# Kernel optimization log

Measured on AMD Instinct MI355X. Metric: run time of the kernel, lower is better.

The kernel has to match this reference:

```python
import jax, jax.numpy as jnp
import numpy as np

B, N, C = 4, 2048, 1024
H = 16
D = C // H  # head_dim = 64
SCALE = 1.0 / np.sqrt(D).astype(np.float32)


def setup_inputs() -> dict:
    key = jax.random.key(0)
    ks = jax.random.split(key, 6)
    s = 0.02
    return {
        "x": jax.random.normal(ks[0], (B, N, C), dtype=jnp.float32),
        "Wq": jax.random.normal(ks[1], (C, C), dtype=jnp.float32) * s,
        "Wk": jax.random.normal(ks[2], (C, C), dtype=jnp.float32) * s,
        "Wv": jax.random.normal(ks[3], (C, C), dtype=jnp.float32) * s,
        "Wo": jax.random.normal(ks[4], (C, C), dtype=jnp.float32) * s,
        "bo": jax.random.normal(ks[5], (C,), dtype=jnp.float32) * s,
    }


def reference(x, Wq, Wk, Wv, Wo, bo):
    # q/k/v projections (no bias, qkv_bias=False), split heads -> [B,H,N,D]
    def heads(t):
        return t.reshape(B, N, H, D).transpose(0, 2, 1, 3)
    q = heads(x @ Wq)
    k = heads(x @ Wk)
    v = heads(x @ Wv)
    attn = jnp.einsum("bhnd,bhmd->bhnm", q, k) * SCALE  # [B,H,N,N]
    attn = jax.nn.softmax(attn, axis=-1)
    out = jnp.einsum("bhnm,bhmd->bhnd", attn, v)  # [B,H,N,D]
    out = out.transpose(0, 2, 1, 3).reshape(B, N, C)
    return out @ Wo + bo
```

## Files before the change

### kernel.cpp

```cpp
#include <hip/hip_runtime.h>
#include <hip/hip_bf16.h>


typedef __bf16 bf16x8 __attribute__((ext_vector_type(8)));
typedef float  f32x4  __attribute__((ext_vector_type(4)));
typedef unsigned int u32x4 __attribute__((ext_vector_type(4)));

__device__ __forceinline__ f32x4 mfma16(bf16x8 a, bf16x8 b, f32x4 c) {
    return __builtin_amdgcn_mfma_f32_16x16x32_bf16(a, b, c, 0, 0, 0);
}

__device__ __forceinline__ unsigned short f2bf(float f) {
    unsigned u = __builtin_bit_cast(unsigned, f);
    u += 0x7fffu + ((u >> 16) & 1u);
    return (unsigned short)(u >> 16);
}

__device__ __forceinline__ unsigned cvt_pk_bf16(float lo, float hi) {
    unsigned r;
    asm("v_cvt_pk_bf16_f32 %0, %1, %2" : "=v"(r) : "v"(lo), "v"(hi));
    return r;
}

__device__ __forceinline__ void gload16(const ushort* g, ushort* l) {
    __builtin_amdgcn_global_load_lds(
        (const __attribute__((address_space(1))) void*)g,
        (__attribute__((address_space(3))) void*)l, 16, 0, 0);
}

__global__ void cast_bf16_kernel(const float4* __restrict__ in,
                                 ushort4* __restrict__ out, int n4) {
    int i = blockIdx.x * blockDim.x + threadIdx.x;
    if (i < n4) {
        float4 f = in[i];
        ushort4 r;
        r.x = f2bf(f.x); r.y = f2bf(f.y); r.z = f2bf(f.z); r.w = f2bf(f.w);
        out[i] = r;
    }
}

__global__ void transpose_cast_kernel(const float* __restrict__ Wq,
                                      const float* __restrict__ Wk,
                                      const float* __restrict__ Wv,
                                      const float* __restrict__ Wo,
                                      ushort* __restrict__ out) {
    __shared__ float tile[32][33];
    const int z = blockIdx.z;
    const float* W = (z == 0) ? Wq : (z == 1) ? Wk : (z == 2) ? Wv : Wo;
    ushort* o = out + (size_t)z * 1024 * 1024;
    const int k0 = blockIdx.x * 32, n0 = blockIdx.y * 32;
    const int tx = threadIdx.x, ty = threadIdx.y;
#pragma unroll
    for (int i = 0; i < 4; i++)
        tile[ty + 8 * i][tx] = W[(size_t)(k0 + ty + 8 * i) * 1024 + n0 + tx];
    __syncthreads();
#pragma unroll
    for (int i = 0; i < 4; i++)
        o[(size_t)(n0 + ty + 8 * i) * 1024 + k0 + tx] = f2bf(tile[tx][ty + 8 * i]);
}

template <int MODE>
__global__ __launch_bounds__(256) void gemm128(const ushort* __restrict__ A,
                                               const ushort* __restrict__ Bt,
                                               ushort* __restrict__ outB,
                                               float* __restrict__ outF,
                                               const float* __restrict__ bias) {
    __shared__ ushort As[128 * 32];
    __shared__ ushort Bs[128 * 32];
    const int tid = threadIdx.x;
    const int lane = tid & 63;
    const int wid = tid >> 6;
    const int wm = wid >> 1, wn = wid & 1;
    const int m0 = blockIdx.x * 128;
    const int n0 = blockIdx.y * 128;
    if (MODE == 0) Bt += (size_t)blockIdx.z * (1024 * 1024);

    f32x4 acc[4][4] = {};

    for (int k0 = 0; k0 < 1024; k0 += 32) {
#pragma unroll
        for (int it = 0; it < 2; ++it) {
            int e = (it * 256 + tid) * 8;
            int r = e >> 5, c = e & 31;
            gload16(&A[(size_t)(m0 + r) * 1024 + k0 + c], &As[e]);
            gload16(&Bt[(size_t)(n0 + r) * 1024 + k0 + c], &Bs[e]);
        }
        __syncthreads();

        bf16x8 a[4], b[4];
#pragma unroll
        for (int i = 0; i < 4; i++) {
            a[i] = *(const bf16x8*)&As[(wm * 64 + i * 16 + (lane & 15)) * 32 + (lane >> 4) * 8];
            b[i] = *(const bf16x8*)&Bs[(wn * 64 + i * 16 + (lane & 15)) * 32 + (lane >> 4) * 8];
        }
#pragma unroll
        for (int i = 0; i < 4; i++)
#pragma unroll
            for (int j = 0; j < 4; j++)
                acc[i][j] = mfma16(a[i], b[j], acc[i][j]);
        __syncthreads();
    }

#pragma unroll
    for (int i = 0; i < 4; i++) {
        int row_b = m0 + wm * 64 + i * 16 + ((lane >> 4) * 4);
#pragma unroll
        for (int j = 0; j < 4; j++) {
            int col = n0 + wn * 64 + j * 16 + (lane & 15);
#pragma unroll
            for (int r = 0; r < 4; r++) {
                int row = row_b + r;
                float v = acc[i][j][r];
                if (MODE == 0) {
                    ushort* o = outB + (size_t)blockIdx.z * (8192ull * 1024);
                    int b = row >> 11, n = row & 2047, h = col >> 6, d = col & 63;
                    o[((((size_t)(b * 16 + h)) * 2048 + n) << 6) + d] = f2bf(v);
                } else {
                    outF[(size_t)row * 1024 + col] = v + bias[col];
                }
            }
        }
    }
}

#define LSCALE 0.18033688f

__global__ __launch_bounds__(256) void attn_kernel(const ushort* __restrict__ Q,
                                                   const ushort* __restrict__ K,
                                                   const ushort* __restrict__ V,
                                                   ushort* __restrict__ O) {
    __shared__ ushort Ks[64 * 64];
    __shared__ ushort Vs[64 * 64];
    __shared__ ushort Ps[4][16 * 64];
    const int tid = threadIdx.x;
    const int lane = tid & 63;
    const int wid = tid >> 6;
    const int g = lane >> 4;
    const int q16 = lane & 15;
    const int qt = blockIdx.x;
    const int bh = blockIdx.y;
    const size_t base = (size_t)bh * (2048 * 64);

    const int qrow = qt * 64 + wid * 16 + q16;
    bf16x8 qf[2];
    qf[0] = *(const bf16x8*)&Q[base + (size_t)qrow * 64 + g * 8];
    qf[1] = *(const bf16x8*)&Q[base + (size_t)qrow * 64 + 32 + g * 8];

    bf16x8 onesb;
#pragma unroll
    for (int i = 0; i < 8; i++) onesb[i] = (__bf16)1.0f;

    f32x4 o[4] = {};
    f32x4 lacc = {};
    float m_run = -1e30f;

    char* KsB = (char*)Ks;
    char* VsB = (char*)Vs;
    char* PsB = (char*)Ps[wid];

    for (int kt = 0; kt < 2048; kt += 64) {
#pragma unroll
        for (int it = 0; it < 2; ++it) {
            int ci = it * 256 + tid;
            int key = ci >> 3, d0 = (ci & 7) * 8;
            uint4 kv = *(const uint4*)&K[base + (size_t)(kt + key) * 64 + d0];
            int byt = (key * 128 + d0 * 2) ^ ((key & 7) << 4);
            *(uint4*)(KsB + byt) = kv;

            int key2 = ci & 63;
            int d0v = (ci >> 6) * 8;
            uint4 vv = *(const uint4*)&V[base + (size_t)(kt + key2) * 64 + d0v];
            const ushort* vs = (const ushort*)&vv;
#pragma unroll
            for (int j = 0; j < 8; j++) {
                int d = d0v + j;
                int b2 = (d * 128 + key2 * 2) ^ ((d & 7) << 4);
                *(ushort*)(VsB + b2) = vs[j];
            }
        }
        __syncthreads();

        f32x4 s[4] = {};
#pragma unroll
        for (int kb = 0; kb < 4; ++kb) {
#pragma unroll
            for (int ks = 0; ks < 2; ++ks) {
                int key = kb * 16 + q16;
                int d0 = ks * 32 + g * 8;
                int byt = (key * 128 + d0 * 2) ^ ((key & 7) << 4);
                bf16x8 kf = *(const bf16x8*)(KsB + byt);
                s[kb] = mfma16(kf, qf[ks], s[kb]);
            }
        }

        float t[4][4];
#pragma unroll
        for (int kb = 0; kb < 4; ++kb)
#pragma unroll
            for (int r = 0; r < 4; ++r) t[kb][r] = s[kb][r] * LSCALE;

        float mx = fmaxf(fmaxf(fmaxf(t[0][0], t[0][1]), fmaxf(t[0][2], t[0][3])),
                         fmaxf(fmaxf(t[1][0], t[1][1]), fmaxf(t[1][2], t[1][3])));
        mx = fmaxf(mx, fmaxf(fmaxf(fmaxf(t[2][0], t[2][1]), fmaxf(t[2][2], t[2][3])),
                             fmaxf(fmaxf(t[3][0], t[3][1]), fmaxf(t[3][2], t[3][3]))));
        mx = fmaxf(mx, __shfl_xor(mx, 16));
        mx = fmaxf(mx, __shfl_xor(mx, 32));
        float mn = fmaxf(m_run, mx);
        float fr = __builtin_amdgcn_exp2f(m_run - mn);
        m_run = mn;

        unsigned w[4][2];
#pragma unroll
        for (int kb = 0; kb < 4; ++kb) {
            float p0 = __builtin_amdgcn_exp2f(t[kb][0] - mn);
            float p1 = __builtin_amdgcn_exp2f(t[kb][1] - mn);
            float p2 = __builtin_amdgcn_exp2f(t[kb][2] - mn);
            float p3 = __builtin_amdgcn_exp2f(t[kb][3] - mn);
            w[kb][0] = cvt_pk_bf16(p0, p1);
            w[kb][1] = cvt_pk_bf16(p2, p3);
        }

        {
            u32x4 c0 = {w[0][0], w[0][1], w[2][0], w[2][1]};
            u32x4 c1 = {w[1][0], w[1][1], w[3][0], w[3][1]};
            *(u32x4*)(PsB + ((lane * 32 + 0)  ^ ((lane & 7) << 4))) = c0;
            *(u32x4*)(PsB + ((lane * 32 + 16) ^ ((lane & 7) << 4))) = c1;
        }
        int s1 = q16 + 32 * (g & 1);
        int ch = (g >> 1) * 16;
        u32x4 r1 = *(const u32x4*)(PsB + ((s1 * 32 + ch) ^ ((s1 & 7) << 4)));
        u32x4 r2 = *(const u32x4*)(PsB + (((s1 + 16) * 32 + ch) ^ (((s1 + 16) & 7) << 4)));
        bf16x8 pa[2];
        {
            u32x4 p0 = {r1.x, r1.y, r2.x, r2.y};
            u32x4 p1 = {r1.z, r1.w, r2.z, r2.w};
            pa[0] = __builtin_bit_cast(bf16x8, p0);
            pa[1] = __builtin_bit_cast(bf16x8, p1);
        }

        float fro[4];
#pragma unroll
        for (int r = 0; r < 4; ++r) fro[r] = __shfl(fr, g * 4 + r);
#pragma unroll
        for (int cb = 0; cb < 4; ++cb)
#pragma unroll
            for (int r = 0; r < 4; ++r) o[cb][r] *= fro[r];
#pragma unroll
        for (int r = 0; r < 4; ++r) lacc[r] *= fro[r];

        lacc = mfma16(pa[0], onesb, lacc);
        lacc = mfma16(pa[1], onesb, lacc);

#pragma unroll
        for (int cb = 0; cb < 4; ++cb) {
#pragma unroll
            for (int ks = 0; ks < 2; ++ks) {
                int d = cb * 16 + q16;
                int byt = (d * 128 + (ks * 32 + g * 8) * 2) ^ ((d & 7) << 4);
                bf16x8 vf = *(const bf16x8*)(VsB + byt);
                o[cb] = mfma16(pa[ks], vf, o[cb]);
            }
        }
        __syncthreads();
    }

    const int b = bh >> 4, h = bh & 15;
#pragma unroll
    for (int r = 0; r < 4; ++r) {
        float inv = 1.0f / lacc[r];
        int row = qt * 64 + wid * 16 + g * 4 + r;
#pragma unroll
        for (int cb = 0; cb < 4; ++cb) {
            int col = h * 64 + cb * 16 + q16;
            O[((size_t)(b * 2048 + row)) * 1024 + col] = f2bf(o[cb][r] * inv);
        }
    }
}

extern "C" void kernel_launch(void* const* d_in, const int* in_sizes, int n_in,
                              void* d_out, int out_size, void* d_ws, size_t ws_size,
                              hipStream_t stream) {
    const float* x  = (const float*)d_in[0];
    const float* Wq = (const float*)d_in[1];
    const float* Wk = (const float*)d_in[2];
    const float* Wv = (const float*)d_in[3];
    const float* Wo = (const float*)d_in[4];
    const float* bo = (const float*)d_in[5];
    float* out = (float*)d_out;

    if (ws_size < (size_t)72 * 1024 * 1024) return;
    ushort* ws  = (ushort*)d_ws;
    ushort* xb  = ws;
    ushort* wt  = xb + (size_t)8 * 1024 * 1024;
    ushort* qkv = wt + (size_t)4 * 1024 * 1024;
    ushort* ao  = xb;

    cast_bf16_kernel<<<8192, 256, 0, stream>>>((const float4*)x, (ushort4*)xb,
                                               2 * 1024 * 1024);
    transpose_cast_kernel<<<dim3(32, 32, 4), dim3(32, 8), 0, stream>>>(Wq, Wk, Wv, Wo, wt);
    gemm128<0><<<dim3(64, 8, 3), 256, 0, stream>>>(xb, wt, qkv, nullptr, nullptr);
    attn_kernel<<<dim3(32, 64), 256, 0, stream>>>(
        qkv, qkv + (size_t)8 * 1024 * 1024, qkv + (size_t)16 * 1024 * 1024, ao);
    gemm128<1><<<dim3(64, 8, 1), 256, 0, stream>>>(ao, wt + (size_t)3 * 1024 * 1024,
                                                   nullptr, out, bo);
}
```

Baseline: 260.0 us.

## Process two 16-row query tiles per wave and swizzle attention block order

Each wave now handles 32 query rows (two 16-row sub-tiles), so every K/V tile staged in shared memory feeds twice as many MFMAs. This halves the number of K/V global loads and LDS staging passes per query row. The grid shrinks to 1024 blocks, and block IDs are remapped so that blocks resident together spread across heads, which is meant to improve cache locality. The cost is more accumulator registers per thread, which may reduce occupancy.

Result: faster. 250.0 us (-3.8%).

```diff
diff --git a/kernel.cpp b/kernel.cpp
--- a/kernel.cpp
+++ b/kernel.cpp
@@ -131,32 +131,36 @@
                                                    ushort* __restrict__ O) {
     __shared__ ushort Ks[64 * 64];
     __shared__ ushort Vs[64 * 64];
-    __shared__ ushort Ps[4][16 * 64];
+    __shared__ ushort Ps[4][2][1024];
     const int tid = threadIdx.x;
     const int lane = tid & 63;
     const int wid = tid >> 6;
     const int g = lane >> 4;
     const int q16 = lane & 15;
-    const int qt = blockIdx.x;
-    const int bh = blockIdx.y;
+    const int bid = blockIdx.x;
+    const int swz = (bid & 7) * 128 + (bid >> 3);
+    const int bh = swz >> 4;
+    const int qt = swz & 15;
     const size_t base = (size_t)bh * (2048 * 64);
 
-    const int qrow = qt * 64 + wid * 16 + q16;
-    bf16x8 qf[2];
-    qf[0] = *(const bf16x8*)&Q[base + (size_t)qrow * 64 + g * 8];
-    qf[1] = *(const bf16x8*)&Q[base + (size_t)qrow * 64 + 32 + g * 8];
+    const int qr0 = qt * 128 + wid * 32 + q16;
+    bf16x8 qf[2][2];
+#pragma unroll
+    for (int u = 0; u < 2; ++u)
+#pragma unroll
+        for (int ks = 0; ks < 2; ++ks)
+            qf[u][ks] = *(const bf16x8*)&Q[base + (size_t)(qr0 + u * 16) * 64 + ks * 32 + g * 8];
 
     bf16x8 onesb;
 #pragma unroll
     for (int i = 0; i < 8; i++) onesb[i] = (__bf16)1.0f;
 
-    f32x4 o[4] = {};
-    f32x4 lacc = {};
-    float m_run = -1e30f;
+    f32x4 o[2][4] = {};
+    f32x4 lacc[2] = {};
+    float m_run[2] = {-1e30f, -1e30f};
 
     char* KsB = (char*)Ks;
     char* VsB = (char*)Vs;
-    char* PsB = (char*)Ps[wid];
 
     for (int kt = 0; kt < 2048; kt += 64) {
 #pragma unroll
@@ -180,7 +184,7 @@
         }
         __syncthreads();
 
-        f32x4 s[4] = {};
+        f32x4 s[2][4] = {};
 #pragma unroll
         for (int kb = 0; kb < 4; ++kb) {
 #pragma unroll
@@ -189,67 +193,75 @@
                 int d0 = ks * 32 + g * 8;
                 int byt = (key * 128 + d0 * 2) ^ ((key & 7) << 4);
                 bf16x8 kf = *(const bf16x8*)(KsB + byt);
-                s[kb] = mfma16(kf, qf[ks], s[kb]);
-            }
-        }
-
-        float t[4][4];
-#pragma unroll
-        for (int kb = 0; kb < 4; ++kb)
-#pragma unroll
-            for (int r = 0; r < 4; ++r) t[kb][r] = s[kb][r] * LSCALE;
-
-        float mx = fmaxf(fmaxf(fmaxf(t[0][0], t[0][1]), fmaxf(t[0][2], t[0][3])),
-                         fmaxf(fmaxf(t[1][0], t[1][1]), fmaxf(t[1][2], t[1][3])));
-        mx = fmaxf(mx, fmaxf(fmaxf(fmaxf(t[2][0], t[2][1]), fmaxf(t[2][2], t[2][3])),
-                             fmaxf(fmaxf(t[3][0], t[3][1]), fmaxf(t[3][2], t[3][3]))));
-        mx = fmaxf(mx, __shfl_xor(mx, 16));
-        mx = fmaxf(mx, __shfl_xor(mx, 32));
-        float mn = fmaxf(m_run, mx);
-        float fr = __builtin_amdgcn_exp2f(m_run - mn);
-        m_run = mn;
-
-        unsigned w[4][2];
-#pragma unroll
-        for (int kb = 0; kb < 4; ++kb) {
-            float p0 = __builtin_amdgcn_exp2f(t[kb][0] - mn);
-            float p1 = __builtin_amdgcn_exp2f(t[kb][1] - mn);
-            float p2 = __builtin_amdgcn_exp2f(t[kb][2] - mn);
-            float p3 = __builtin_amdgcn_exp2f(t[kb][3] - mn);
-            w[kb][0] = cvt_pk_bf16(p0, p1);
-            w[kb][1] = cvt_pk_bf16(p2, p3);
-        }
-
-        {
-            u32x4 c0 = {w[0][0], w[0][1], w[2][0], w[2][1]};
-            u32x4 c1 = {w[1][0], w[1][1], w[3][0], w[3][1]};
-            *(u32x4*)(PsB + ((lane * 32 + 0)  ^ ((lane & 7) << 4))) = c0;
-            *(u32x4*)(PsB + ((lane * 32 + 16) ^ ((lane & 7) << 4))) = c1;
-        }
-        int s1 = q16 + 32 * (g & 1);
-        int ch = (g >> 1) * 16;
-        u32x4 r1 = *(const u32x4*)(PsB + ((s1 * 32 + ch) ^ ((s1 & 7) << 4)));
-        u32x4 r2 = *(const u32x4*)(PsB + (((s1 + 16) * 32 + ch) ^ (((s1 + 16) & 7) << 4)));
-        bf16x8 pa[2];
-        {
-            u32x4 p0 = {r1.x, r1.y, r2.x, r2.y};
-            u32x4 p1 = {r1.z, r1.w, r2.z, r2.w};
-            pa[0] = __builtin_bit_cast(bf16x8, p0);
-            pa[1] = __builtin_bit_cast(bf16x8, p1);
-        }
-
-        float fro[4];
-#pragma unroll
-        for (int r = 0; r < 4; ++r) fro[r] = __shfl(fr, g * 4 + r);
-#pragma unroll
-        for (int cb = 0; cb < 4; ++cb)
-#pragma unroll
-            for (int r = 0; r < 4; ++r) o[cb][r] *= fro[r];
-#pragma unroll
-        for (int r = 0; r < 4; ++r) lacc[r] *= fro[r];
-
-        lacc = mfma16(pa[0], onesb, lacc);
-        lacc = mfma16(pa[1], onesb, lacc);
+                s[0][kb] = mfma16(kf, qf[0][ks], s[0][kb]);
+                s[1][kb] = mfma16(kf, qf[1][ks], s[1][kb]);
+            }
+        }
+
+        bf16x8 pa[2][2];
+#pragma unroll
+        for (int u = 0; u < 2; ++u) {
+            float t[4][4];
+#pragma unroll
+            for (int kb = 0; kb < 4; ++kb)
+#pragma unroll
+                for (int r = 0; r < 4; ++r) t[kb][r] = s[u][kb][r] * LSCALE;
+
+            float mx = fmaxf(fmaxf(fmaxf(t[0][0], t[0][1]), fmaxf(t[0][2], t[0][3])),
+                             fmaxf(fmaxf(t[1][0], t[1][1]), fmaxf(t[1][2], t[1][3])));
+            mx = fmaxf(mx, fmaxf(fmaxf(fmaxf(t[2][0], t[2][1]), fmaxf(t[2][2], t[2][3])),
+                                 fmaxf(fmaxf(t[3][0], t[3][1]), fmaxf(t[3][2], t[3][3]))));
+            mx = fmaxf(mx, __shfl_xor(mx, 16));
+            mx = fmaxf(mx, __shfl_xor(mx, 32));
+            float mn = fmaxf(m_run[u], mx);
+            float fr = __builtin_amdgcn_exp2f(m_run[u] - mn);
+            m_run[u] = mn;
+
+            unsigned w[4][2];
+#pragma unroll
+            for (int kb = 0; kb < 4; ++kb) {
+                float p0 = __builtin_amdgcn_exp2f(t[kb][0] - mn);
+                float p1 = __builtin_amdgcn_exp2f(t[kb][1] - mn);
+                float p2 = __builtin_amdgcn_exp2f(t[kb][2] - mn);
+                float p3 = __builtin_amdgcn_exp2f(t[kb][3] - mn);
+                w[kb][0] = cvt_pk_bf16(p0, p1);
+                w[kb][1] = cvt_pk_bf16(p2, p3);
+            }
+
+            char* PsB = (char*)Ps[wid][u];
+            {
+                u32x4 c0 = {w[0][0], w[0][1], w[2][0], w[2][1]};
+                u32x4 c1 = {w[1][0], w[1][1], w[3][0], w[3][1]};
+                *(u32x4*)(PsB + ((lane * 32 + 0)  ^ ((lane & 7) << 4))) = c0;
+                *(u32x4*)(PsB + ((lane * 32 + 16) ^ ((lane & 7) << 4))) = c1;
+            }
+            asm volatile("" ::: "memory");
+            __builtin_amdgcn_sched_barrier(0);
+            int s1 = q16 + 32 * (g & 1);
+            int ch = (g >> 1) * 16;
+            u32x4 r1 = *(const u32x4*)(PsB + ((s1 * 32 + ch) ^ ((s1 & 7) << 4)));
+            u32x4 r2 = *(const u32x4*)(PsB + (((s1 + 16) * 32 + ch) ^ (((s1 + 16) & 7) << 4)));
+            asm volatile("" ::: "memory");
+            {
+                u32x4 p0 = {r1.x, r1.y, r2.x, r2.y};
+                u32x4 p1 = {r1.z, r1.w, r2.z, r2.w};
+                pa[u][0] = __builtin_bit_cast(bf16x8, p0);
+                pa[u][1] = __builtin_bit_cast(bf16x8, p1);
+            }
+
+            float fro[4];
+#pragma unroll
+            for (int r = 0; r < 4; ++r) fro[r] = __shfl(fr, g * 4 + r);
+#pragma unroll
+            for (int cb = 0; cb < 4; ++cb)
+#pragma unroll
+                for (int r = 0; r < 4; ++r) o[u][cb][r] *= fro[r];
+#pragma unroll
+            for (int r = 0; r < 4; ++r) lacc[u][r] *= fro[r];
+
+            lacc[u] = mfma16(pa[u][0], onesb, lacc[u]);
+            lacc[u] = mfma16(pa[u][1], onesb, lacc[u]);
+        }
 
 #pragma unroll
         for (int cb = 0; cb < 4; ++cb) {
@@ -258,7 +270,8 @@
                 int d = cb * 16 + q16;
                 int byt = (d * 128 + (ks * 32 + g * 8) * 2) ^ ((d & 7) << 4);
                 bf16x8 vf = *(const bf16x8*)(VsB + byt);
-                o[cb] = mfma16(pa[ks], vf, o[cb]);
+                o[0][cb] = mfma16(pa[0][ks], vf, o[0][cb]);
+                o[1][cb] = mfma16(pa[1][ks], vf, o[1][cb]);
             }
         }
         __syncthreads();
@@ -266,13 +279,16 @@
 
     const int b = bh >> 4, h = bh & 15;
 #pragma unroll
-    for (int r = 0; r < 4; ++r) {
-        float inv = 1.0f / lacc[r];
-        int row = qt * 64 + wid * 16 + g * 4 + r;
-#pragma unroll
-        for (int cb = 0; cb < 4; ++cb) {
-            int col = h * 64 + cb * 16 + q16;
-            O[((size_t)(b * 2048 + row)) * 1024 + col] = f2bf(o[cb][r] * inv);
+    for (int u = 0; u < 2; ++u) {
+#pragma unroll
+        for (int r = 0; r < 4; ++r) {
+            float inv = 1.0f / lacc[u][r];
+            int row = qt * 128 + wid * 32 + u * 16 + g * 4 + r;
+#pragma unroll
+            for (int cb = 0; cb < 4; ++cb) {
+                int col = h * 64 + cb * 16 + q16;
+                O[((size_t)(b * 2048 + row)) * 1024 + col] = f2bf(o[u][cb][r] * inv);
+            }
         }
     }
 }
@@ -299,7 +315,7 @@
                                                2 * 1024 * 1024);
     transpose_cast_kernel<<<dim3(32, 32, 4), dim3(32, 8), 0, stream>>>(Wq, Wk, Wv, Wo, wt);
     gemm128<0><<<dim3(64, 8, 3), 256, 0, stream>>>(xb, wt, qkv, nullptr, nullptr);
-    attn_kernel<<<dim3(32, 64), 256, 0, stream>>>(
+    attn_kernel<<<1024, 256, 0, stream>>>(
         qkv, qkv + (size_t)8 * 1024 * 1024, qkv + (size_t)16 * 1024 * 1024, ao);
     gemm128<1><<<dim3(64, 8, 1), 256, 0, stream>>>(ao, wt + (size_t)3 * 1024 * 1024,
                                                    nullptr, out, bo);
```
